# Kernel optimization log

Measured on AMD Instinct MI355X. Metric: run time of the kernel, lower is better.

Reference implementation:

```python
import jax, jax.numpy as jnp
import numpy as np

N = 8192

def setup_inputs() -> dict:
    key = jax.random.key(0)
    k1, k2 = jax.random.split(key)
    estimated_adj = jax.random.uniform(k1, (N, N), dtype=jnp.float32)
    ori = jax.random.uniform(k2, (N, N), dtype=jnp.float32)
    return {"estimated_adj": estimated_adj, "ori": ori}

def reference(estimated_adj, ori):
    # normalize(): adj = estimated_adj * ori; mx = adj + I; row-normalize.
    n = estimated_adj.shape[0]
    mx = estimated_adj * ori + jnp.eye(n, dtype=estimated_adj.dtype)
    rowsum = mx.sum(axis=1)  # [n]
    r_inv = jnp.power(rowsum, -1.0)
    r_inv = jnp.where(jnp.isinf(r_inv), 0.0, r_inv)
    # diag(r_inv) @ mx is mathematically a per-row scale; do it without the O(n^3) GEMM.
    return r_inv[:, None] * mx
```

## Files before the change

kernel.cpp:

```cpp
#include <hip/hip_runtime.h>
#include <math.h>


#define NDIM 8192
#define BLOCK 512
#define V4_PER_THREAD (NDIM / 4 / BLOCK)
#define WAVES (BLOCK / 64)

typedef float f32x4 __attribute__((ext_vector_type(4)));

__global__ __launch_bounds__(BLOCK, 8) void row_normalize_kernel(
    const float* __restrict__ a,
    const float* __restrict__ b,
    float* __restrict__ out)
{
    __shared__ f32x4 stash[NDIM / 4];
    __shared__ double wave_sums[WAVES];

    const int row = blockIdx.x;
    const int tid = threadIdx.x;

    const f32x4* __restrict__ a4 = (const f32x4*)(a + (size_t)row * NDIM);
    const f32x4* __restrict__ b4 = (const f32x4*)(b + (size_t)row * NDIM);
    f32x4*       __restrict__ o4 = (f32x4*)(out + (size_t)row * NDIM);

    f32x4 av[V4_PER_THREAD], bv[V4_PER_THREAD];
#pragma unroll
    for (int i = 0; i < V4_PER_THREAD; ++i)
        av[i] = a4[tid + i * BLOCK];
#pragma unroll
    for (int i = 0; i < V4_PER_THREAD; ++i)
        bv[i] = b4[tid + i * BLOCK];

    double sum = 0.0;
#pragma unroll
    for (int i = 0; i < V4_PER_THREAD; ++i) {
        const int idx = tid + i * BLOCK;
        f32x4 p = av[i] * bv[i];
        const int col0 = idx << 2;
        if ((unsigned)(row - col0) < 4u) {
            if      (row == col0)     p.x += 1.0f;
            else if (row == col0 + 1) p.y += 1.0f;
            else if (row == col0 + 2) p.z += 1.0f;
            else                      p.w += 1.0f;
        }
        stash[idx] = p;
        sum += (double)p.x + (double)p.y + (double)p.z + (double)p.w;
    }

#pragma unroll
    for (int off = 32; off > 0; off >>= 1)
        sum += __shfl_down(sum, off, 64);

    const int lane = tid & 63;
    const int wave = tid >> 6;
    if (lane == 0) wave_sums[wave] = sum;
    __syncthreads();

    double total = 0.0;
#pragma unroll
    for (int w = 0; w < WAVES; ++w) total += wave_sums[w];
    float r_inv = 1.0f / (float)total;
    if (isinf(r_inv)) r_inv = 0.0f;

#pragma unroll
    for (int i = 0; i < V4_PER_THREAD; ++i) {
        const int idx = tid + i * BLOCK;
        f32x4 p = stash[idx];
        p *= r_inv;
        o4[idx] = p;
    }
}

extern "C" void kernel_launch(void* const* d_in, const int* in_sizes, int n_in,
                              void* d_out, int out_size, void* d_ws, size_t ws_size,
                              hipStream_t stream) {
    const float* a = (const float*)d_in[0];
    const float* b = (const float*)d_in[1];
    float* out = (float*)d_out;
    row_normalize_kernel<<<NDIM, BLOCK, 0, stream>>>(a, b, out);
}
```

Before: 582.0 us.

## Load rows directly into LDS via global_load_lds and double block size

Each row of both inputs is now copied into shared memory with the global-to-LDS direct load instruction (16 bytes per lane, 1 KB chunks split across waves) instead of through registers, and the block grows from 512 to 1024 threads. The goal is to cut register pressure and keep more loads in flight. The cost is 64 KB of LDS per block, which allows only one block per CU at a time, plus an extra barrier and LDS reads before compute.

After: 580.4 us. Within noise of the previous version (-0.3%).

```diff
diff --git a/kernel.cpp b/kernel.cpp
--- a/kernel.cpp
+++ b/kernel.cpp
@@ -3,40 +3,55 @@
 
 
 #define NDIM 8192
-#define BLOCK 512
+#define BLOCK 1024
+#define WAVES (BLOCK / 64)
 #define V4_PER_THREAD (NDIM / 4 / BLOCK)
-#define WAVES (BLOCK / 64)
+#define ROW_BYTES (NDIM * 4)
+#define CHUNK_BYTES 1024
+#define CHUNKS (ROW_BYTES / CHUNK_BYTES)
+#define CHUNKS_PER_WAVE (CHUNKS / WAVES)
 
 typedef float f32x4 __attribute__((ext_vector_type(4)));
+typedef __attribute__((address_space(3))) unsigned int lds_u32;
+typedef const __attribute__((address_space(1))) unsigned int glb_u32;
+
+__device__ __forceinline__ void dma16(const void* g, void* lds) {
+    __builtin_amdgcn_global_load_lds((glb_u32*)g, (lds_u32*)lds, 16, 0, 0);
+}
 
 __global__ __launch_bounds__(BLOCK, 8) void row_normalize_kernel(
     const float* __restrict__ a,
     const float* __restrict__ b,
     float* __restrict__ out)
 {
-    __shared__ f32x4 stash[NDIM / 4];
+    __shared__ f32x4 bufA[NDIM / 4];
+    __shared__ f32x4 bufB[NDIM / 4];
     __shared__ double wave_sums[WAVES];
 
-    const int row = blockIdx.x;
-    const int tid = threadIdx.x;
+    const int row  = blockIdx.x;
+    const int tid  = threadIdx.x;
+    const int lane = tid & 63;
+    const int wave = tid >> 6;
 
-    const f32x4* __restrict__ a4 = (const f32x4*)(a + (size_t)row * NDIM);
-    const f32x4* __restrict__ b4 = (const f32x4*)(b + (size_t)row * NDIM);
-    f32x4*       __restrict__ o4 = (f32x4*)(out + (size_t)row * NDIM);
+    const char* arow = (const char*)(a + (size_t)row * NDIM);
+    const char* brow = (const char*)(b + (size_t)row * NDIM);
+    f32x4* __restrict__ o4 = (f32x4*)(out + (size_t)row * NDIM);
 
-    f32x4 av[V4_PER_THREAD], bv[V4_PER_THREAD];
 #pragma unroll
-    for (int i = 0; i < V4_PER_THREAD; ++i)
-        av[i] = a4[tid + i * BLOCK];
-#pragma unroll
-    for (int i = 0; i < V4_PER_THREAD; ++i)
-        bv[i] = b4[tid + i * BLOCK];
+    for (int k = 0; k < CHUNKS_PER_WAVE; ++k) {
+        const int c = wave * CHUNKS_PER_WAVE + k;
+        const int goff = c * CHUNK_BYTES + lane * 16;
+        dma16(arow + goff, (char*)bufA + c * CHUNK_BYTES);
+        dma16(brow + goff, (char*)bufB + c * CHUNK_BYTES);
+    }
+    asm volatile("s_waitcnt vmcnt(0)" ::: "memory");
+    __syncthreads();
 
     double sum = 0.0;
 #pragma unroll
     for (int i = 0; i < V4_PER_THREAD; ++i) {
         const int idx = tid + i * BLOCK;
-        f32x4 p = av[i] * bv[i];
+        f32x4 p = bufA[idx] * bufB[idx];
         const int col0 = idx << 2;
         if ((unsigned)(row - col0) < 4u) {
             if      (row == col0)     p.x += 1.0f;
@@ -44,7 +59,7 @@
             else if (row == col0 + 2) p.z += 1.0f;
             else                      p.w += 1.0f;
         }
-        stash[idx] = p;
+        bufA[idx] = p;
         sum += (double)p.x + (double)p.y + (double)p.z + (double)p.w;
     }
 
@@ -52,8 +67,6 @@
     for (int off = 32; off > 0; off >>= 1)
         sum += __shfl_down(sum, off, 64);
 
-    const int lane = tid & 63;
-    const int wave = tid >> 6;
     if (lane == 0) wave_sums[wave] = sum;
     __syncthreads();
 
@@ -66,7 +79,7 @@
 #pragma unroll
     for (int i = 0; i < V4_PER_THREAD; ++i) {
         const int idx = tid + i * BLOCK;
-        f32x4 p = stash[idx];
+        f32x4 p = bufA[idx];
         p *= r_inv;
         o4[idx] = p;
     }
```
